# Kernel tuning notes

Measured on AMD Instinct MI355X. Metric: run time of the kernel, lower is better.

## Reference

```python
import jax, jax.numpy as jnp
import numpy as np

NUM_GROUPS = 32
EPS = 1e-5
HT_MIN = -1.0
HT_MAX = 1.0


def setup_inputs() -> dict:
    key = jax.random.key(0)
    k1, k2, k3 = jax.random.split(key, 3)
    B, IN, OUT = 8192, 2048, 4096
    x = jax.random.normal(k1, (B, IN), dtype=jnp.float32)
    # kaiming-uniform-ish scale for weight, uniform bias in [-1/sqrt(fan_in), 1/sqrt(fan_in)]
    bound_w = np.sqrt(1.0 / IN)
    weight = jax.random.uniform(k2, (OUT, IN), dtype=jnp.float32, minval=-bound_w, maxval=bound_w)
    bias = jax.random.uniform(k3, (OUT,), dtype=jnp.float32, minval=-bound_w, maxval=bound_w)
    return {"x": x, "weight": weight, "bias": bias}


def reference(x, weight, bias):
    # GEMM + bias: (B, out)
    y = jnp.einsum('bi,oi->bo', x, weight) + bias
    B, OUT = y.shape
    fpg = OUT // NUM_GROUPS
    g = y.reshape(B, NUM_GROUPS, fpg)
    mean = jnp.mean(g, axis=-1, keepdims=True)
    var = jnp.mean(jnp.square(g - mean), axis=-1, keepdims=True)  # biased variance
    x_hat = (g - mean) / jnp.sqrt(var + EPS)
    out = jnp.clip(x_hat, HT_MIN, HT_MAX)
    return out.reshape(B, OUT)
```

## Files before the change

kernel.cpp:

```cpp
#include <hip/hip_runtime.h>
#include <hip/hip_bf16.h>

#define B_ROWS   8192
#define K_DIM    2048
#define OUT_COLS 4096
#define EPS      1e-5f

#define BM 128
#define BN 256
#define BK 32
#define NKT (K_DIM / BK)

using f32x4  = __attribute__((ext_vector_type(4))) float;
using bf16x8 = __attribute__((ext_vector_type(8))) short;

__device__ __forceinline__ unsigned short f2bf_rn(float f) {
    unsigned u = __builtin_bit_cast(unsigned, f);
    u += 0x7FFFu + ((u >> 16) & 1u);
    return (unsigned short)(u >> 16);
}

__global__ void cvt_all(const float* __restrict__ x, const float* __restrict__ w,
                        unsigned short* __restrict__ xb, unsigned short* __restrict__ wb) {
    const int n4x = (B_ROWS * K_DIM) / 4;
    const int n4w = (OUT_COLS * K_DIM) / 4;
    int stride = gridDim.x * blockDim.x;
    for (int i = blockIdx.x * blockDim.x + threadIdx.x; i < n4x + n4w; i += stride) {
        const float4* src; ushort4* dst; int j;
        if (i < n4x) { src = (const float4*)x; dst = (ushort4*)xb; j = i; }
        else         { src = (const float4*)w; dst = (ushort4*)wb; j = i - n4x; }
        float4 v = src[j];
        ushort4 r;
        r.x = f2bf_rn(v.x); r.y = f2bf_rn(v.y); r.z = f2bf_rn(v.z); r.w = f2bf_rn(v.w);
        dst[j] = r;
    }
}

__device__ __forceinline__ void gload16(const unsigned short* src, unsigned short* lds) {
    __builtin_amdgcn_global_load_lds((const __attribute__((address_space(1))) void*)src,
                                     (__attribute__((address_space(3))) void*)lds,
                                     16, 0, 0);
}

__device__ __forceinline__ float rowsum16(float v) {
    int x;
    x = __builtin_amdgcn_update_dpp(0, __builtin_bit_cast(int, v), 0x121, 0xF, 0xF, true);
    v += __builtin_bit_cast(float, x);
    x = __builtin_amdgcn_update_dpp(0, __builtin_bit_cast(int, v), 0x122, 0xF, 0xF, true);
    v += __builtin_bit_cast(float, x);
    x = __builtin_amdgcn_update_dpp(0, __builtin_bit_cast(int, v), 0x124, 0xF, 0xF, true);
    v += __builtin_bit_cast(float, x);
    x = __builtin_amdgcn_update_dpp(0, __builtin_bit_cast(int, v), 0x128, 0xF, 0xF, true);
    v += __builtin_bit_cast(float, x);
    return v;
}

#define VW3   asm volatile("s_waitcnt vmcnt(3)" ::: "memory")
#define VWALL asm volatile("s_waitcnt vmcnt(0)" ::: "memory")
#define BAR   __builtin_amdgcn_s_barrier()

#define STAGE(AOFF, BOFF, KT) do {                                                  \
    gload16(Ag + (KT)*32 + goffA,  &As[(AOFF) + ldsA]);                             \
    gload16(Bg + (KT)*32 + goffB0, &Bs[(BOFF) + ldsB0]);                            \
    gload16(Bg + (KT)*32 + goffB1, &Bs[(BOFF) + ldsB1]);                            \
  } while (0)

#define KTILE(AOFF, BOFF, SAOFF, SBOFF, KT2) do {                                   \
    bf16x8 af[4], bb[4];                                                            \
    STAGE(SAOFF, SBOFF, KT2);                                                       \
    _Pragma("unroll") for (int m = 0; m < 4; ++m)                                   \
        af[m] = *(const bf16x8*)&As[(AOFF) + arow + m*512 + csw];                   \
    _Pragma("unroll") for (int n = 0; n < 4; ++n)                                   \
        bb[n] = *(const bf16x8*)&Bs[(BOFF) + brw + n*512 + csw];                    \
    __builtin_amdgcn_s_setprio(1);                                                  \
    _Pragma("unroll") for (int m = 0; m < 4; ++m)                                   \
      _Pragma("unroll") for (int n = 0; n < 4; ++n)                                 \
        acc[m][n] = __builtin_amdgcn_mfma_f32_16x16x32_bf16(                        \
            af[m], bb[n], acc[m][n], 0, 0, 0);                                      \
    __builtin_amdgcn_s_setprio(0);                                                  \
    VW3;                                                                            \
    BAR;                                                                            \
  } while (0)

__global__ __launch_bounds__(512, 4) void gemm_gn(const unsigned short* __restrict__ A,
                                                  const unsigned short* __restrict__ Bw,
                                                  const float* __restrict__ bias,
                                                  float* __restrict__ out) {
    __shared__ __align__(16) unsigned short As[3 * 4096];
    __shared__ __align__(16) unsigned short Bs[3 * 8192];
    __shared__ __align__(16) float redbuf[128 * 8];

    const int tid  = threadIdx.x;
    const int lane = tid & 63;
    const int wave = tid >> 6;
    const int wr   = wave >> 2;
    const int wcn  = wave & 3;
    const int l16  = lane & 15;
    const int lhi  = lane >> 4;

    const int bid  = blockIdx.x;
    const int swz  = (bid & 7) * (gridDim.x >> 3) + (bid >> 3);
    const int brow = swz >> 4;
    const int bcol = swz & 15;

    int goffA, ldsA, goffB0, goffB1, ldsB0, ldsB1;
    {
        int sA = tid;              int rA = sA >> 2;
        goffA  = rA * K_DIM + (((sA & 3) ^ ((rA >> 1) & 3)) * 8);
        ldsA   = sA * 8;
        int s0 = tid;              int r0 = s0 >> 2;
        int s1 = tid + 512;        int r1 = s1 >> 2;
        goffB0 = r0 * K_DIM + (((s0 & 3) ^ ((r0 >> 1) & 3)) * 8);
        goffB1 = r1 * K_DIM + (((s1 & 3) ^ ((r1 >> 1) & 3)) * 8);
        ldsB0  = s0 * 8;
        ldsB1  = s1 * 8;
    }
    const unsigned short* Ag = A  + (size_t)brow * BM * K_DIM;
    const unsigned short* Bg = Bw + (size_t)bcol * BN * K_DIM;

    const int csw  = (lhi ^ ((l16 >> 1) & 3)) * 8;
    const int arow = (wr * 64 + l16) * 32;
    const int brw  = (wcn * 64 + l16) * 32;

    f32x4 acc[4][4];
    {
        float bv[4];
        #pragma unroll
        for (int n = 0; n < 4; ++n)
            bv[n] = bias[bcol * BN + wcn * 64 + n * 16 + l16];
        #pragma unroll
        for (int m = 0; m < 4; ++m)
            #pragma unroll
            for (int n = 0; n < 4; ++n)
                #pragma unroll
                for (int j = 0; j < 4; ++j)
                    acc[m][n][j] = bv[n];
    }

    STAGE(0, 0, 0);
    STAGE(4096, 8192, 1);
    VW3;
    BAR;

    #pragma unroll 1
    for (int it = 0; it < 21; ++it) {
        const int kt = it * 3;
        KTILE(0,    0,     8192, 16384, kt + 2);
        KTILE(4096, 8192,  0,    0,     kt + 3);
        KTILE(8192, 16384, 4096, 8192,  (kt + 4) & 63);
    }
    {
        bf16x8 af[4], bb[4];
        #pragma unroll
        for (int m = 0; m < 4; ++m)
            af[m] = *(const bf16x8*)&As[arow + m*512 + csw];
        #pragma unroll
        for (int n = 0; n < 4; ++n)
            bb[n] = *(const bf16x8*)&Bs[brw + n*512 + csw];
        #pragma unroll
        for (int m = 0; m < 4; ++m)
            #pragma unroll
            for (int n = 0; n < 4; ++n)
                acc[m][n] = __builtin_amdgcn_mfma_f32_16x16x32_bf16(
                    af[m], bb[n], acc[m][n], 0, 0, 0);
    }

    #pragma unroll
    for (int m = 0; m < 4; ++m) {
        #pragma unroll
        for (int j = 0; j < 4; ++j) {
            float s = 0.f, s2 = 0.f;
            #pragma unroll
            for (int n = 0; n < 4; ++n) {
                float v = acc[m][n][j];
                s += v; s2 += v * v;
            }
            s  = rowsum16(s);
            s2 = rowsum16(s2);
            if (l16 == 0) {
                int r = wr * 64 + m * 16 + lhi * 4 + j;
                redbuf[r * 8 + wcn * 2 + 0] = s;
                redbuf[r * 8 + wcn * 2 + 1] = s2;
            }
        }
    }
    VWALL;
    __syncthreads();

    const int p2 = (wcn & 2) * 2;
    #pragma unroll
    for (int m = 0; m < 4; ++m) {
        #pragma unroll
        for (int j = 0; j < 4; ++j) {
            const int r = wr * 64 + m * 16 + lhi * 4 + j;
            const float4 q = *(const float4*)&redbuf[r * 8 + p2];
            const float mean = (q.x + q.z) * (1.0f / 128.0f);
            const float var  = (q.y + q.w) * (1.0f / 128.0f) - mean * mean;
            const float rstd = rsqrtf(var + EPS);
            float* orow = out + (size_t)(brow * BM + r) * OUT_COLS + bcol * BN + wcn * 64 + l16;
            #pragma unroll
            for (int n = 0; n < 4; ++n) {
                float v = (acc[m][n][j] - mean) * rstd;
                v = fminf(fmaxf(v, -1.0f), 1.0f);
                orow[n * 16] = v;
            }
        }
    }
}

extern "C" void kernel_launch(void* const* d_in, const int* in_sizes, int n_in,
                              void* d_out, int out_size, void* d_ws, size_t ws_size,
                              hipStream_t stream) {
    const float* x    = (const float*)d_in[0];
    const float* w    = (const float*)d_in[1];
    const float* bias = (const float*)d_in[2];
    float* out        = (float*)d_out;

    unsigned short* xb = (unsigned short*)d_ws;
    unsigned short* wb = xb + (size_t)B_ROWS * K_DIM;

    cvt_all<<<3072, 256, 0, stream>>>(x, w, xb, wb);

    dim3 grid((B_ROWS / BM) * (OUT_COLS / BN));
    gemm_gn<<<grid, 512, 0, stream>>>(xb, wb, bias, out);
}
```

Before: 182.1 us.

## Enlarge GEMM block tile to 256x256x64 with 16 waves and double buffering

Restructures the fused GEMM+GroupNorm kernel so each 1024-thread block computes a 256x256 output tile with a K-step of 64. Shared-memory staging changes from triple-buffered 32-wide K slices to two 64-wide buffers, with a new XOR swizzle. Each K tile runs two MFMA phases, then a full vmcnt wait and a barrier. This raises data reuse per loaded byte and halves the number of barriers. In exchange it needs about 136 KB of LDS per block, loses the partial-wait prefetch overlap, and the launch_bounds(1024,4) hint may squeeze the register budget.

```diff
diff --git a/kernel.cpp b/kernel.cpp
--- a/kernel.cpp
+++ b/kernel.cpp
@@ -6,10 +6,10 @@
 #define OUT_COLS 4096
 #define EPS      1e-5f
 
-#define BM 128
+#define BM 256
 #define BN 256
-#define BK 32
-#define NKT (K_DIM / BK)
+#define BK 64
+#define NT (K_DIM / BK)
 
 using f32x4  = __attribute__((ext_vector_type(4))) float;
 using bf16x8 = __attribute__((ext_vector_type(8))) short;
@@ -55,40 +55,42 @@
     return v;
 }
 
-#define VW3   asm volatile("s_waitcnt vmcnt(3)" ::: "memory")
 #define VWALL asm volatile("s_waitcnt vmcnt(0)" ::: "memory")
 #define BAR   __builtin_amdgcn_s_barrier()
 
-#define STAGE(AOFF, BOFF, KT) do {                                                  \
-    gload16(Ag + (KT)*32 + goffA,  &As[(AOFF) + ldsA]);                             \
-    gload16(Bg + (KT)*32 + goffB0, &Bs[(BOFF) + ldsB0]);                            \
-    gload16(Bg + (KT)*32 + goffB1, &Bs[(BOFF) + ldsB1]);                            \
-  } while (0)
-
-#define KTILE(AOFF, BOFF, SAOFF, SBOFF, KT2) do {                                   \
+#define STA(BUF, H, KT) gload16(Ag + (H)*262144 + (KT)*64 + goffA, &As[BUF][(H)*8192 + ldsA])
+#define STB(BUF, H, KT) gload16(Bg + (H)*262144 + (KT)*64 + goffA, &Bs[BUF][(H)*8192 + ldsA])
+
+#define PHASE(BUF, CSW) do {                                                        \
     bf16x8 af[4], bb[4];                                                            \
-    STAGE(SAOFF, SBOFF, KT2);                                                       \
     _Pragma("unroll") for (int m = 0; m < 4; ++m)                                   \
-        af[m] = *(const bf16x8*)&As[(AOFF) + arow + m*512 + csw];                   \
+        af[m] = *(const bf16x8*)&As[BUF][abase + m*1024 + (CSW)];                   \
     _Pragma("unroll") for (int n = 0; n < 4; ++n)                                   \
-        bb[n] = *(const bf16x8*)&Bs[(BOFF) + brw + n*512 + csw];                    \
+        bb[n] = *(const bf16x8*)&Bs[BUF][bbase + n*1024 + (CSW)];                   \
     __builtin_amdgcn_s_setprio(1);                                                  \
     _Pragma("unroll") for (int m = 0; m < 4; ++m)                                   \
       _Pragma("unroll") for (int n = 0; n < 4; ++n)                                 \
         acc[m][n] = __builtin_amdgcn_mfma_f32_16x16x32_bf16(                        \
             af[m], bb[n], acc[m][n], 0, 0, 0);                                      \
     __builtin_amdgcn_s_setprio(0);                                                  \
-    VW3;                                                                            \
+  } while (0)
+
+#define KTILE(BUF, NB, KTN) do {                                                    \
+    STA(NB, 0, KTN); STA(NB, 1, KTN);                                               \
+    STB(NB, 0, KTN); STB(NB, 1, KTN);                                               \
+    PHASE(BUF, csw0);                                                               \
+    PHASE(BUF, csw1);                                                               \
+    VWALL;                                                                          \
     BAR;                                                                            \
   } while (0)
 
-__global__ __launch_bounds__(512, 4) void gemm_gn(const unsigned short* __restrict__ A,
-                                                  const unsigned short* __restrict__ Bw,
-                                                  const float* __restrict__ bias,
-                                                  float* __restrict__ out) {
-    __shared__ __align__(16) unsigned short As[3 * 4096];
-    __shared__ __align__(16) unsigned short Bs[3 * 8192];
-    __shared__ __align__(16) float redbuf[128 * 8];
+__global__ __launch_bounds__(1024, 4) void gemm_gn(const unsigned short* __restrict__ A,
+                                                   const unsigned short* __restrict__ Bw,
+                                                   const float* __restrict__ bias,
+                                                   float* __restrict__ out) {
+    __shared__ __align__(16) unsigned short As[2][16384];
+    __shared__ __align__(16) unsigned short Bs[2][16384];
+    __shared__ __align__(16) float redbuf[256 * 8];
 
     const int tid  = threadIdx.x;
     const int lane = tid & 63;
@@ -103,24 +105,19 @@
     const int brow = swz >> 4;
     const int bcol = swz & 15;
 
-    int goffA, ldsA, goffB0, goffB1, ldsB0, ldsB1;
+    int goffA, ldsA;
     {
-        int sA = tid;              int rA = sA >> 2;
-        goffA  = rA * K_DIM + (((sA & 3) ^ ((rA >> 1) & 3)) * 8);
-        ldsA   = sA * 8;
-        int s0 = tid;              int r0 = s0 >> 2;
-        int s1 = tid + 512;        int r1 = s1 >> 2;
-        goffB0 = r0 * K_DIM + (((s0 & 3) ^ ((r0 >> 1) & 3)) * 8);
-        goffB1 = r1 * K_DIM + (((s1 & 3) ^ ((r1 >> 1) & 3)) * 8);
-        ldsB0  = s0 * 8;
-        ldsB1  = s1 * 8;
+        int s = tid;  int r = s >> 3;
+        goffA = r * K_DIM + (((s & 7) ^ (r & 7)) * 8);
+        ldsA  = s * 8;
     }
     const unsigned short* Ag = A  + (size_t)brow * BM * K_DIM;
     const unsigned short* Bg = Bw + (size_t)bcol * BN * K_DIM;
 
-    const int csw  = (lhi ^ ((l16 >> 1) & 3)) * 8;
-    const int arow = (wr * 64 + l16) * 32;
-    const int brw  = (wcn * 64 + l16) * 32;
+    const int csw0  = ((0 * 4 + lhi) ^ (l16 & 7)) * 8;
+    const int csw1  = ((1 * 4 + lhi) ^ (l16 & 7)) * 8;
+    const int abase = (wr >> 1) * 8192 + ((wr & 1) * 64 + l16) * 64;
+    const int bbase = (wcn >> 1) * 8192 + ((wcn & 1) * 64 + l16) * 64;
 
     f32x4 acc[4][4];
     {
@@ -137,32 +134,16 @@
                     acc[m][n][j] = bv[n];
     }
 
-    STAGE(0, 0, 0);
-    STAGE(4096, 8192, 1);
-    VW3;
+    STA(0, 0, 0); STA(0, 1, 0);
+    STB(0, 0, 0); STB(0, 1, 0);
+    VWALL;
     BAR;
 
     #pragma unroll 1
-    for (int it = 0; it < 21; ++it) {
-        const int kt = it * 3;
-        KTILE(0,    0,     8192, 16384, kt + 2);
-        KTILE(4096, 8192,  0,    0,     kt + 3);
-        KTILE(8192, 16384, 4096, 8192,  (kt + 4) & 63);
-    }
-    {
-        bf16x8 af[4], bb[4];
-        #pragma unroll
-        for (int m = 0; m < 4; ++m)
-            af[m] = *(const bf16x8*)&As[arow + m*512 + csw];
-        #pragma unroll
-        for (int n = 0; n < 4; ++n)
-            bb[n] = *(const bf16x8*)&Bs[brw + n*512 + csw];
-        #pragma unroll
-        for (int m = 0; m < 4; ++m)
-            #pragma unroll
-            for (int n = 0; n < 4; ++n)
-                acc[m][n] = __builtin_amdgcn_mfma_f32_16x16x32_bf16(
-                    af[m], bb[n], acc[m][n], 0, 0, 0);
+    for (int it = 0; it < NT / 2; ++it) {
+        const int kt = it * 2;
+        KTILE(0, 1, kt + 1);
+        KTILE(1, 0, (kt + 2) & (NT - 1));
     }
 
     #pragma unroll
@@ -184,7 +165,6 @@
             }
         }
     }
-    VWALL;
     __syncthreads();
 
     const int p2 = (wcn & 2) * 2;
@@ -222,5 +202,5 @@
     cvt_all<<<3072, 256, 0, stream>>>(x, w, xb, wb);
 
     dim3 grid((B_ROWS / BM) * (OUT_COLS / BN));
-    gemm_gn<<<grid, 512, 0, stream>>>(xb, wb, bias, out);
-}
+    gemm_gn<<<grid, 1024, 0, stream>>>(xb, wb, bias, out);
+}
```

Result: faster. 155.4 us (median of 2 runs) (-14.7%).
